# Kernel optimization log

Hardware: AMD Instinct MI355X
Metric: run time of the kernel (lower is better)

Reference implementation:

```python
import jax, jax.numpy as jnp
import numpy as np

B, D, T = 32, 1024, 1000
LMAX = 200
VOCAB = 80
BLANK = VOCAB - 1
NEG = -1e30


def setup_inputs() -> dict:
    key = jax.random.key(0)
    ks = jax.random.split(key, 8)
    decoder_outputs = jax.random.normal(ks[0], (B, D, T), dtype=jnp.float32)
    target_text = jax.random.randint(ks[1], (B, LMAX), 0, BLANK, dtype=jnp.int32)
    decoder_lengths = jax.random.randint(ks[2], (B,), T // 2, T + 1, dtype=jnp.int32)
    target_lengths = jax.random.randint(ks[3], (B,), 1, LMAX + 1, dtype=jnp.int32)
    # learned params (dropout is identity in eval / deterministic reference)
    W1 = jax.random.normal(ks[4], (D, D), dtype=jnp.float32) * (1.0 / np.sqrt(D))
    b1 = jnp.zeros((D,), dtype=jnp.float32)
    W2 = jax.random.normal(ks[5], (D, VOCAB), dtype=jnp.float32) * (1.0 / np.sqrt(D))
    b2 = jnp.zeros((VOCAB,), dtype=jnp.float32)
    return {"decoder_outputs": decoder_outputs, "target_text": target_text,
            "decoder_lengths": decoder_lengths, "target_lengths": target_lengths,
            "W1": W1, "b1": b1, "W2": W2, "b2": b2}


def _ctc_nll(log_probs, targets, input_lengths, target_lengths):
    # log_probs: [T, B, V]; standard CTC alpha (forward) DP over extended labels.
    Tt, Bb, V = log_probs.shape
    L = targets.shape[1]
    S = 2 * L + 1
    ext = jnp.full((Bb, S), BLANK, dtype=targets.dtype).at[:, 1::2].set(targets)
    ext_m2 = jnp.pad(ext, ((0, 0), (2, 0)), constant_values=BLANK)[:, :S]
    allow_skip = (ext != BLANK) & (ext != ext_m2)
    allow_skip = allow_skip.at[:, :2].set(False)

    lp0 = log_probs[0]  # [B, V]
    alpha0 = jnp.full((Bb, S), NEG, dtype=log_probs.dtype)
    alpha0 = alpha0.at[:, 0].set(lp0[:, BLANK])
    alpha0 = alpha0.at[:, 1].set(jnp.take_along_axis(lp0, targets[:, :1], axis=1)[:, 0])

    def step(alpha, inp):
        lp_t, t = inp
        emit = jnp.take_along_axis(lp_t, ext, axis=1)  # [B, S]
        a2 = jnp.pad(alpha, ((0, 0), (1, 0)), constant_values=NEG)[:, :S]
        a3 = jnp.pad(alpha, ((0, 0), (2, 0)), constant_values=NEG)[:, :S]
        a3 = jnp.where(allow_skip, a3, NEG)
        new = jnp.logaddexp(jnp.logaddexp(alpha, a2), a3) + emit
        alpha = jnp.where((t < input_lengths)[:, None], new, alpha)
        return alpha, None

    alpha, _ = jax.lax.scan(step, alpha0, (log_probs[1:], jnp.arange(1, Tt)))
    i1 = (2 * target_lengths - 1)[:, None]
    i2 = (2 * target_lengths)[:, None]
    last = jnp.logaddexp(jnp.take_along_axis(alpha, i1, axis=1)[:, 0],
                         jnp.take_along_axis(alpha, i2, axis=1)[:, 0])
    nll = -last
    # zero_infinity=True: invalid alignments -> 0 loss
    return jnp.where(last > NEG / 2, nll, 0.0)


def reference(decoder_outputs, target_text, decoder_lengths, target_lengths, W1, b1, W2, b2):
    x = jnp.transpose(decoder_outputs, (0, 2, 1))          # [B, T, D]
    h = jax.nn.relu(jnp.einsum('btd,de->bte', x, W1) + b1)  # proj + ReLU (dropout=identity)
    logits = jnp.einsum('btd,dv->btv', h, W2) + b2          # [B, T, V]
    log_probs = jax.nn.log_softmax(logits, axis=2)
    log_probs = jnp.transpose(log_probs, (1, 0, 2))         # [T, B, V]
    ctc_loss = _ctc_nll(log_probs, target_text, decoder_lengths, target_lengths)
    return (ctc_loss / decoder_lengths.astype(jnp.float32)).mean()
```

## Files before the change

kernel.cpp:

```cpp
#include <hip/hip_runtime.h>
#include <cstdint>
#include <cstddef>

#define BN_ 32
#define DD_ 1024
#define TT_ 1000
#define LMAX_ 200
#define VC_ 80
#define BLANK_ 79
#define SS_ 401
#define SPAD 512
#define NEGV (-1e30f)

typedef _Float16 half8 __attribute__((ext_vector_type(8)));
typedef float f32x4 __attribute__((ext_vector_type(4)));

__device__ __forceinline__ void async16(const void* g, void* l) {
  __builtin_amdgcn_global_load_lds(
      (const __attribute__((address_space(1))) unsigned int*)g,
      (__attribute__((address_space(3))) unsigned int*)l, 16, 0, 0);
}

__global__ void transpose_cast_kernel(const float* __restrict__ in,
                                      _Float16* __restrict__ out,
                                      int R, int C) {
  __shared__ float tile[32][33];
  size_t bo = (size_t)blockIdx.z * R * C;
  int c0 = blockIdx.x * 32, r0 = blockIdx.y * 32;
  int tx = threadIdx.x, ty = threadIdx.y;
#pragma unroll
  for (int k = 0; k < 32; k += 8) {
    int r = r0 + ty + k, c = c0 + tx;
    if (r < R && c < C) tile[ty + k][tx] = in[bo + (size_t)r * C + c];
  }
  __syncthreads();
#pragma unroll
  for (int k = 0; k < 32; k += 8) {
    int c = c0 + ty + k, r = r0 + tx;
    if (c < C && r < R) out[bo + (size_t)c * R + r] = (_Float16)tile[tx][ty + k];
  }
}

__global__ __launch_bounds__(256) void gemm_relu_kernel(
    const _Float16* __restrict__ A, const _Float16* __restrict__ Bt,
    const float* __restrict__ bias, _Float16* __restrict__ H,
    int M, int N, int K) {
  constexpr int BK = 64;
  __shared__ __align__(16) _Float16 sA[128 * BK];
  __shared__ __align__(16) _Float16 sB[128 * BK];
  int tid = threadIdx.x;
  int wave = tid >> 6, lane = tid & 63;
  int quad = lane >> 4, r16 = lane & 15;
  int m0 = blockIdx.y * 128, n0 = blockIdx.x * 128;
  int moff = (wave >> 1) * 64, noff = (wave & 1) * 64;

  f32x4 acc[4][4];
#pragma unroll
  for (int i = 0; i < 4; ++i)
#pragma unroll
    for (int j = 0; j < 4; ++j) acc[i][j] = {0.f, 0.f, 0.f, 0.f};

  for (int kt = 0; kt < K; kt += BK) {
#pragma unroll
    for (int jj = 0; jj < 4; ++jj) {
      int seg = tid + 256 * jj;
      int row = seg >> 3, slot = seg & 7;
      int cg = slot ^ (row & 7);
      async16(A + (size_t)(m0 + row) * K + kt + cg * 8, &sA[seg * 8]);
      async16(Bt + (size_t)(n0 + row) * K + kt + cg * 8, &sB[seg * 8]);
    }
    __syncthreads();
#pragma unroll
    for (int ku = 0; ku < 2; ++ku) {
      int sw = ((ku * 4 + quad) ^ (r16 & 7)) * 8;
      half8 af[4], bfr[4];
#pragma unroll
      for (int i = 0; i < 4; ++i)
        af[i] = *(const half8*)&sA[(moff + i * 16 + r16) * BK + sw];
#pragma unroll
      for (int j = 0; j < 4; ++j)
        bfr[j] = *(const half8*)&sB[(noff + j * 16 + r16) * BK + sw];
#pragma unroll
      for (int i = 0; i < 4; ++i)
#pragma unroll
        for (int j = 0; j < 4; ++j)
          acc[i][j] = __builtin_amdgcn_mfma_f32_16x16x32_f16(af[i], bfr[j], acc[i][j], 0, 0, 0);
    }
    __syncthreads();
  }
#pragma unroll
  for (int j = 0; j < 4; ++j) {
    int n = n0 + noff + j * 16 + r16;
    float bv = bias[n];
#pragma unroll
    for (int i = 0; i < 4; ++i) {
#pragma unroll
      for (int r = 0; r < 4; ++r) {
        int m = m0 + moff + i * 16 + quad * 4 + r;
        float v = acc[i][j][r] + bv;
        v = fmaxf(v, 0.f);
        H[(size_t)m * N + n] = (_Float16)v;
      }
    }
  }
}

__global__ __launch_bounds__(256) void gemm_lsm_kernel(
    const _Float16* __restrict__ A, const _Float16* __restrict__ Bt,
    const float* __restrict__ bias, float* __restrict__ LP, int M, int K) {
  constexpr int BK = 64;
  __shared__ __align__(16) _Float16 sA[128 * BK];
  __shared__ __align__(16) _Float16 sB[VC_ * BK];
  int tid = threadIdx.x;
  int wave = tid >> 6, lane = tid & 63;
  int quad = lane >> 4, r16 = lane & 15;
  int m0 = blockIdx.x * 128;

  f32x4 acc[2][5];
#pragma unroll
  for (int i = 0; i < 2; ++i)
#pragma unroll
    for (int j = 0; j < 5; ++j) acc[i][j] = {0.f, 0.f, 0.f, 0.f};

  for (int kt = 0; kt < K; kt += BK) {
#pragma unroll
    for (int jj = 0; jj < 4; ++jj) {
      int seg = tid + 256 * jj;
      int row = seg >> 3, slot = seg & 7;
      int cg = slot ^ (row & 7);
      async16(A + (size_t)(m0 + row) * K + kt + cg * 8, &sA[seg * 8]);
    }
#pragma unroll
    for (int jj = 0; jj < 3; ++jj) {
      int seg = tid + 256 * jj;
      if (seg < VC_ * 8) {
        int row = seg >> 3, slot = seg & 7;
        int cg = slot ^ (row & 7);
        async16(Bt + (size_t)row * K + kt + cg * 8, &sB[seg * 8]);
      }
    }
    __syncthreads();
#pragma unroll
    for (int ku = 0; ku < 2; ++ku) {
      int sw = ((ku * 4 + quad) ^ (r16 & 7)) * 8;
      half8 af[2], bfr[5];
#pragma unroll
      for (int i = 0; i < 2; ++i)
        af[i] = *(const half8*)&sA[(wave * 32 + i * 16 + r16) * BK + sw];
#pragma unroll
      for (int j = 0; j < 5; ++j)
        bfr[j] = *(const half8*)&sB[(j * 16 + r16) * BK + sw];
#pragma unroll
      for (int i = 0; i < 2; ++i)
#pragma unroll
        for (int j = 0; j < 5; ++j)
          acc[i][j] = __builtin_amdgcn_mfma_f32_16x16x32_f16(af[i], bfr[j], acc[i][j], 0, 0, 0);
    }
    __syncthreads();
  }
  float bv[5];
#pragma unroll
  for (int j = 0; j < 5; ++j) bv[j] = bias[j * 16 + r16];
#pragma unroll
  for (int i = 0; i < 2; ++i) {
#pragma unroll
    for (int rr = 0; rr < 4; ++rr) {
      float vals[5];
      float mx = -3.4e38f;
#pragma unroll
      for (int j = 0; j < 5; ++j) {
        vals[j] = acc[i][j][rr] + bv[j];
        mx = fmaxf(mx, vals[j]);
      }
#pragma unroll
      for (int d = 1; d < 16; d <<= 1) mx = fmaxf(mx, __shfl_xor(mx, d));
      float sm = 0.f;
#pragma unroll
      for (int j = 0; j < 5; ++j) sm += expf(vals[j] - mx);
#pragma unroll
      for (int d = 1; d < 16; d <<= 1) sm += __shfl_xor(sm, d);
      float lse = mx + logf(sm);
      int m = m0 + wave * 32 + i * 16 + quad * 4 + rr;
      float* o = LP + (size_t)m * VC_;
#pragma unroll
      for (int j = 0; j < 5; ++j) o[j * 16 + r16] = vals[j] - lse;
    }
  }
}

__global__ __launch_bounds__(256) void emit_kernel(
    const float* __restrict__ LP, const int* __restrict__ targets,
    float* __restrict__ EM) {
  int idx = blockIdx.x * 256 + threadIdx.x;
  int s = idx & (SPAD - 1);
  int bt = idx >> 9;
  float v = 0.f;
  if (s < SS_) {
    int lab = BLANK_;
    if (s & 1) {
      int b = bt / TT_;
      lab = targets[b * LMAX_ + (s >> 1)];
    }
    v = __expf(LP[(size_t)bt * VC_ + lab]);
  }
  EM[idx] = v;
}

__device__ __forceinline__ void dp_step_fwd(float (&bta)[8], int& k,
                                            const f32x4 e0, const f32x4 e1,
                                            const float (&am)[4], int lane) {
  float pm1 = __shfl_up(bta[7], 1);
  int pk = __shfl_up(k, 1);
  if (lane == 0) { pm1 = 0.f; pk = k; }
  int knew = max(k, pk);
  pm1 = ldexpf(pm1, pk - knew);
  int ds = k - knew;
#pragma unroll
  for (int r = 0; r < 8; ++r) bta[r] = ldexpf(bta[r], ds);
  k = knew;
  float nb[8];
  nb[0] = (bta[0] + pm1) * e0.x;
  nb[1] = fmaf(am[0], pm1, bta[1] + bta[0]) * e0.y;
  nb[2] = (bta[2] + bta[1]) * e0.z;
  nb[3] = fmaf(am[1], bta[1], bta[3] + bta[2]) * e0.w;
  nb[4] = (bta[4] + bta[3]) * e1.x;
  nb[5] = fmaf(am[2], bta[3], bta[5] + bta[4]) * e1.y;
  nb[6] = (bta[6] + bta[5]) * e1.z;
  nb[7] = fmaf(am[3], bta[5], bta[7] + bta[6]) * e1.w;
#pragma unroll
  for (int r = 0; r < 8; ++r) bta[r] = nb[r];
}

__device__ __forceinline__ void dp_step_bwd(float (&g)[8], int& k,
                                            const f32x4 e0, const f32x4 e1,
                                            const float (&amB)[4], int lane) {
  float gh[8];
  gh[0] = g[0] * e0.x; gh[1] = g[1] * e0.y;
  gh[2] = g[2] * e0.z; gh[3] = g[3] * e0.w;
  gh[4] = g[4] * e1.x; gh[5] = g[5] * e1.y;
  gh[6] = g[6] * e1.z; gh[7] = g[7] * e1.w;
  float qm1 = __shfl_down(gh[0], 1);
  float qm2 = __shfl_down(gh[1], 1);
  int nk = __shfl_down(k, 1);
  if (lane == 63) { qm1 = 0.f; qm2 = 0.f; nk = k; }
  int knew = max(k, nk);
  int dq = nk - knew;
  qm1 = ldexpf(qm1, dq);
  qm2 = ldexpf(qm2, dq);
  int ds = k - knew;
#pragma unroll
  for (int r = 0; r < 8; ++r) gh[r] = ldexpf(gh[r], ds);
  k = knew;
  g[0] = gh[0] + gh[1];
  g[1] = fmaf(amB[0], gh[3], gh[1] + gh[2]);
  g[2] = gh[2] + gh[3];
  g[3] = fmaf(amB[1], gh[5], gh[3] + gh[4]);
  g[4] = gh[4] + gh[5];
  g[5] = fmaf(amB[2], gh[7], gh[5] + gh[6]);
  g[6] = gh[6] + gh[7];
  g[7] = fmaf(amB[3], qm2, gh[7] + qm1);
}

__device__ __forceinline__ void dp_rescale(float (&v)[8], int& k) {
  float m = fmaxf(fmaxf(fmaxf(v[0], v[1]), fmaxf(v[2], v[3])),
                  fmaxf(fmaxf(v[4], v[5]), fmaxf(v[6], v[7])));
  int ex = (__float_as_int(m) >> 23) - 126;
  k += ex;
#pragma unroll
  for (int r = 0; r < 8; ++r) v[r] = ldexpf(v[r], -ex);
}

__device__ __forceinline__ float allow_f(const int* __restrict__ tg, int s) {
  if (!(s & 1) || s < 3) return 0.f;
  int li = s >> 1;
  if (li >= LMAX_) return 0.f;
  int lab = tg[li];
  return (lab != BLANK_ && lab != tg[li - 1]) ? 1.f : 0.f;
}

__global__ __launch_bounds__(128) void ctc_dp_kernel(
    const float* __restrict__ EM, const int* __restrict__ targets,
    const int* __restrict__ dlen, const int* __restrict__ tlen,
    float* __restrict__ partial) {
  __shared__ float sg[SPAD];
  __shared__ int skg[64];
  int b = blockIdx.x;
  int wave = threadIdx.x >> 6;
  int lane = threadIdx.x & 63;
  const float* em = EM + (size_t)b * TT_ * SPAD + lane * 8;
  const int* tg = targets + b * LMAX_;
  int Tl = dlen[b], Ll = tlen[b];
  int tm = Tl >> 1;

  constexpr int PD = 8;
  f32x4 pf[PD][2];
  float v[8];
  int k = 0;

  if (wave == 0) {
    float am[4];
#pragma unroll
    for (int j = 0; j < 4; ++j) am[j] = allow_f(tg, lane * 8 + 2 * j + 1);
    f32x4 r0a = *(const f32x4*)(em);
#pragma unroll
    for (int r = 0; r < 8; ++r) v[r] = 0.f;
    if (lane == 0) { v[0] = r0a.x; v[1] = r0a.y; }
#pragma unroll
    for (int j = 0; j < PD; ++j) {
      int ri = min(1 + j, TT_ - 1);
      pf[j][0] = *(const f32x4*)(em + (size_t)ri * SPAD);
      pf[j][1] = *(const f32x4*)(em + (size_t)ri * SPAD + 4);
    }
    int t = 1;
    for (; t + (PD - 1) <= tm; t += PD) {
#pragma unroll
      for (int u = 0; u < PD; ++u) {
        dp_step_fwd(v, k, pf[u][0], pf[u][1], am, lane);
        if (u & 1) dp_rescale(v, k);
        int ri = min(t + u + PD, TT_ - 1);
        pf[u][0] = *(const f32x4*)(em + (size_t)ri * SPAD);
        pf[u][1] = *(const f32x4*)(em + (size_t)ri * SPAD + 4);
      }
    }
#pragma unroll
    for (int u = 0; u < PD; ++u) {
      if (t + u <= tm) {
        dp_step_fwd(v, k, pf[u][0], pf[u][1], am, lane);
        if (u & 1) dp_rescale(v, k);
      }
    }
  } else {
    float amB[4];
#pragma unroll
    for (int j = 0; j < 4; ++j) amB[j] = allow_f(tg, lane * 8 + 2 * j + 3);
    int s1 = 2 * Ll - 1, s2 = 2 * Ll;
#pragma unroll
    for (int r = 0; r < 8; ++r) {
      int s = lane * 8 + r;
      v[r] = (s == s1 || s == s2) ? 1.f : 0.f;
    }
#pragma unroll
    for (int j = 0; j < PD; ++j) {
      int ri = max(Tl - 1 - j, 0);
      pf[j][0] = *(const f32x4*)(em + (size_t)ri * SPAD);
      pf[j][1] = *(const f32x4*)(em + (size_t)ri * SPAD + 4);
    }
    int t = Tl - 1;
    for (; t - (PD - 1) > tm; t -= PD) {
#pragma unroll
      for (int u = 0; u < PD; ++u) {
        dp_step_bwd(v, k, pf[u][0], pf[u][1], amB, lane);
        if (u & 1) dp_rescale(v, k);
        int ri = max(t - u - PD, 0);
        pf[u][0] = *(const f32x4*)(em + (size_t)ri * SPAD);
        pf[u][1] = *(const f32x4*)(em + (size_t)ri * SPAD + 4);
      }
    }
#pragma unroll
    for (int u = 0; u < PD; ++u) {
      if (t - u > tm) {
        dp_step_bwd(v, k, pf[u][0], pf[u][1], amB, lane);
        if (u & 1) dp_rescale(v, k);
      }
    }
#pragma unroll
    for (int r = 0; r < 8; ++r) sg[lane * 8 + r] = v[r];
    skg[lane] = k;
  }
  __syncthreads();
  if (wave == 0) {
    float p = 0.f;
#pragma unroll
    for (int r = 0; r < 8; ++r) p = fmaf(v[r], sg[lane * 8 + r], p);
    int kk = k + skg[lane];
    if (p == 0.f) kk = -(1 << 30);
#pragma unroll
    for (int d = 1; d < 64; d <<= 1) {
      float po = __shfl_xor(p, d);
      int ko = __shfl_xor(kk, d);
      int km = max(kk, ko);
      p = ldexpf(p, kk - km) + ldexpf(po, ko - km);
      kk = km;
    }
    if (lane == 0) {
      float nll = 0.f;
      if (p > 0.f) nll = -((log2f(p) + (float)kk) * 0.69314718055994531f);
      partial[b] = nll / (float)Tl;
    }
  }
}

__global__ void finalize_kernel(const float* __restrict__ partial,
                                float* __restrict__ out) {
  int l = threadIdx.x;
  float v = (l < BN_) ? partial[l] : 0.f;
#pragma unroll
  for (int d = 1; d < 64; d <<= 1) v += __shfl_xor(v, d);
  if (l == 0) out[0] = v * (1.f / BN_);
}

extern "C" void kernel_launch(void* const* d_in, const int* in_sizes, int n_in,
                              void* d_out, int out_size, void* d_ws, size_t ws_size,
                              hipStream_t stream) {
  const float* dec = (const float*)d_in[0];
  const int* tgt   = (const int*)d_in[1];
  const int* dln   = (const int*)d_in[2];
  const int* tln   = (const int*)d_in[3];
  const float* W1  = (const float*)d_in[4];
  const float* b1  = (const float*)d_in[5];
  const float* W2  = (const float*)d_in[6];
  const float* b2  = (const float*)d_in[7];
  float* out = (float*)d_out;

  char* ws = (char*)d_ws;
  const size_t M = (size_t)BN_ * TT_;
  _Float16* Af   = (_Float16*)(ws);
  float* EM      = (float*)(ws);
  _Float16* Hf   = (_Float16*)(ws + 65536000);
  _Float16* W1T  = (_Float16*)(ws + 131072000);
  _Float16* W2T  = (_Float16*)(ws + 133169152);
  float* LPp     = (float*)(ws + 133332992);
  float* partial = (float*)(ws + 143572992);

  dim3 tb(32, 8, 1);
  transpose_cast_kernel<<<dim3((TT_ + 31) / 32, DD_ / 32, BN_), tb, 0, stream>>>(dec, Af, DD_, TT_);
  transpose_cast_kernel<<<dim3(DD_ / 32, DD_ / 32, 1), tb, 0, stream>>>(W1, W1T, DD_, DD_);
  transpose_cast_kernel<<<dim3((VC_ + 31) / 32, DD_ / 32, 1), tb, 0, stream>>>(W2, W2T, DD_, VC_);

  gemm_relu_kernel<<<dim3(DD_ / 128, M / 128, 1), 256, 0, stream>>>(
      Af, W1T, b1, Hf, (int)M, DD_, DD_);
  gemm_lsm_kernel<<<dim3(M / 128, 1, 1), 256, 0, stream>>>(
      Hf, W2T, b2, LPp, (int)M, DD_);
  emit_kernel<<<dim3((BN_ * TT_ * SPAD) / 256, 1, 1), 256, 0, stream>>>(LPp, tgt, EM);
  ctc_dp_kernel<<<dim3(BN_, 1, 1), 128, 0, stream>>>(EM, tgt, dln, tln, partial);
  finalize_kernel<<<1, 64, 0, stream>>>(partial, out);
}
```

Before: 453.5 us.

## Merge transposes, shrink LSM GEMM tile, emit probabilities, fold finalize into atomics

```diff
diff --git a/kernel.cpp b/kernel.cpp
--- a/kernel.cpp
+++ b/kernel.cpp
@@ -21,23 +21,43 @@
       (__attribute__((address_space(3))) unsigned int*)l, 16, 0, 0);
 }
 
-__global__ void transpose_cast_kernel(const float* __restrict__ in,
-                                      _Float16* __restrict__ out,
-                                      int R, int C) {
-  __shared__ float tile[32][33];
-  size_t bo = (size_t)blockIdx.z * R * C;
-  int c0 = blockIdx.x * 32, r0 = blockIdx.y * 32;
-  int tx = threadIdx.x, ty = threadIdx.y;
-#pragma unroll
-  for (int k = 0; k < 32; k += 8) {
-    int r = r0 + ty + k, c = c0 + tx;
-    if (r < R && c < C) tile[ty + k][tx] = in[bo + (size_t)r * C + c];
-  }
+__global__ __launch_bounds__(256) void transpose_all_kernel(
+    const float* __restrict__ dec, const float* __restrict__ W1,
+    const float* __restrict__ W2, _Float16* __restrict__ Af,
+    _Float16* __restrict__ W1T, _Float16* __restrict__ W2T) {
+  __shared__ _Float16 T[64][72];
+  int z = blockIdx.z;
+  const float* in; _Float16* out; int C;
+  const int R = 1024;
+  if (z < 32) {
+    in = dec + (size_t)z * R * TT_;
+    out = Af + (size_t)z * TT_ * R;
+    C = TT_;
+  } else if (z == 32) {
+    in = W1; out = W1T; C = 1024;
+  } else {
+    in = W2; out = W2T; C = VC_;
+  }
+  int c0 = blockIdx.x * 64, r0 = blockIdx.y * 64;
+  if (c0 >= C) return;
+  int tid = threadIdx.x;
+  int cl = tid & 63, rg = tid >> 6;
+  int c = c0 + cl;
+  bool cv = (c < C);
+  const float* ip = in + (size_t)(r0 + rg * 16) * C + c;
+  _Float16 h[16];
+#pragma unroll
+  for (int i = 0; i < 16; ++i) h[i] = cv ? (_Float16)ip[(size_t)i * C] : (_Float16)0.f;
+  *(half8*)&T[cl][rg * 16] = *(half8*)&h[0];
+  *(half8*)&T[cl][rg * 16 + 8] = *(half8*)&h[8];
   __syncthreads();
-#pragma unroll
-  for (int k = 0; k < 32; k += 8) {
-    int c = c0 + ty + k, r = r0 + tx;
-    if (c < C && r < R) out[bo + (size_t)c * R + r] = (_Float16)tile[tx][ty + k];
+  int cr = tid >> 2, rc = (tid & 3) * 16;
+  if (c0 + cr < C) {
+    half8 a = *(const half8*)&T[cr][rc];
+    half8 b2 = *(const half8*)&T[cr][rc + 8];
+    _Float16* op = out + (size_t)(c0 + cr) * R + r0 + rc;
+    *(half8*)op = a;
+    *(half8*)(op + 8) = b2;
   }
 }
 
@@ -105,26 +125,24 @@
   }
 }
 
-__global__ __launch_bounds__(256) void gemm_lsm_kernel(
+__global__ __launch_bounds__(256) void gemm_prob_kernel(
     const _Float16* __restrict__ A, const _Float16* __restrict__ Bt,
-    const float* __restrict__ bias, float* __restrict__ LP, int M, int K) {
+    const float* __restrict__ bias, float* __restrict__ P, int M, int K) {
   constexpr int BK = 64;
-  __shared__ __align__(16) _Float16 sA[128 * BK];
+  __shared__ __align__(16) _Float16 sA[64 * BK];
   __shared__ __align__(16) _Float16 sB[VC_ * BK];
   int tid = threadIdx.x;
   int wave = tid >> 6, lane = tid & 63;
   int quad = lane >> 4, r16 = lane & 15;
-  int m0 = blockIdx.x * 128;
-
-  f32x4 acc[2][5];
-#pragma unroll
-  for (int i = 0; i < 2; ++i)
-#pragma unroll
-    for (int j = 0; j < 5; ++j) acc[i][j] = {0.f, 0.f, 0.f, 0.f};
+  int m0 = blockIdx.x * 64;
+
+  f32x4 acc[5];
+#pragma unroll
+  for (int j = 0; j < 5; ++j) acc[j] = {0.f, 0.f, 0.f, 0.f};
 
   for (int kt = 0; kt < K; kt += BK) {
 #pragma unroll
-    for (int jj = 0; jj < 4; ++jj) {
+    for (int jj = 0; jj < 2; ++jj) {
       int seg = tid + 256 * jj;
       int row = seg >> 3, slot = seg & 7;
       int cg = slot ^ (row & 7);
@@ -143,18 +161,14 @@
 #pragma unroll
     for (int ku = 0; ku < 2; ++ku) {
       int sw = ((ku * 4 + quad) ^ (r16 & 7)) * 8;
-      half8 af[2], bfr[5];
-#pragma unroll
-      for (int i = 0; i < 2; ++i)
-        af[i] = *(const half8*)&sA[(wave * 32 + i * 16 + r16) * BK + sw];
+      half8 af = *(const half8*)&sA[(wave * 16 + r16) * BK + sw];
+      half8 bfr[5];
 #pragma unroll
       for (int j = 0; j < 5; ++j)
         bfr[j] = *(const half8*)&sB[(j * 16 + r16) * BK + sw];
 #pragma unroll
-      for (int i = 0; i < 2; ++i)
-#pragma unroll
-        for (int j = 0; j < 5; ++j)
-          acc[i][j] = __builtin_amdgcn_mfma_f32_16x16x32_f16(af[i], bfr[j], acc[i][j], 0, 0, 0);
+      for (int j = 0; j < 5; ++j)
+        acc[j] = __builtin_amdgcn_mfma_f32_16x16x32_f16(af, bfr[j], acc[j], 0, 0, 0);
     }
     __syncthreads();
   }
@@ -162,34 +176,31 @@
 #pragma unroll
   for (int j = 0; j < 5; ++j) bv[j] = bias[j * 16 + r16];
 #pragma unroll
-  for (int i = 0; i < 2; ++i) {
-#pragma unroll
-    for (int rr = 0; rr < 4; ++rr) {
-      float vals[5];
-      float mx = -3.4e38f;
-#pragma unroll
-      for (int j = 0; j < 5; ++j) {
-        vals[j] = acc[i][j][rr] + bv[j];
-        mx = fmaxf(mx, vals[j]);
-      }
-#pragma unroll
-      for (int d = 1; d < 16; d <<= 1) mx = fmaxf(mx, __shfl_xor(mx, d));
-      float sm = 0.f;
-#pragma unroll
-      for (int j = 0; j < 5; ++j) sm += expf(vals[j] - mx);
-#pragma unroll
-      for (int d = 1; d < 16; d <<= 1) sm += __shfl_xor(sm, d);
-      float lse = mx + logf(sm);
-      int m = m0 + wave * 32 + i * 16 + quad * 4 + rr;
-      float* o = LP + (size_t)m * VC_;
-#pragma unroll
-      for (int j = 0; j < 5; ++j) o[j * 16 + r16] = vals[j] - lse;
-    }
+  for (int rr = 0; rr < 4; ++rr) {
+    float vals[5];
+    float mx = -3.4e38f;
+#pragma unroll
+    for (int j = 0; j < 5; ++j) {
+      vals[j] = acc[j][rr] + bv[j];
+      mx = fmaxf(mx, vals[j]);
+    }
+#pragma unroll
+    for (int d = 1; d < 16; d <<= 1) mx = fmaxf(mx, __shfl_xor(mx, d));
+    float ex[5], sm = 0.f;
+#pragma unroll
+    for (int j = 0; j < 5; ++j) { ex[j] = __expf(vals[j] - mx); sm += ex[j]; }
+#pragma unroll
+    for (int d = 1; d < 16; d <<= 1) sm += __shfl_xor(sm, d);
+    float rinv = 1.f / sm;
+    int m = m0 + wave * 16 + quad * 4 + rr;
+    float* o = P + (size_t)m * VC_;
+#pragma unroll
+    for (int j = 0; j < 5; ++j) o[j * 16 + r16] = ex[j] * rinv;
   }
 }
 
 __global__ __launch_bounds__(256) void emit_kernel(
-    const float* __restrict__ LP, const int* __restrict__ targets,
+    const float* __restrict__ P, const int* __restrict__ targets,
     float* __restrict__ EM) {
   int idx = blockIdx.x * 256 + threadIdx.x;
   int s = idx & (SPAD - 1);
@@ -201,7 +212,7 @@
       int b = bt / TT_;
       lab = targets[b * LMAX_ + (s >> 1)];
     }
-    v = __expf(LP[(size_t)bt * VC_ + lab]);
+    v = P[(size_t)bt * VC_ + lab];
   }
   EM[idx] = v;
 }
@@ -281,7 +292,7 @@
 __global__ __launch_bounds__(128) void ctc_dp_kernel(
     const float* __restrict__ EM, const int* __restrict__ targets,
     const int* __restrict__ dlen, const int* __restrict__ tlen,
-    float* __restrict__ partial) {
+    float* __restrict__ out) {
   __shared__ float sg[SPAD];
   __shared__ int skg[64];
   int b = blockIdx.x;
@@ -385,18 +396,9 @@
     if (lane == 0) {
       float nll = 0.f;
       if (p > 0.f) nll = -((log2f(p) + (float)kk) * 0.69314718055994531f);
-      partial[b] = nll / (float)Tl;
-    }
-  }
-}
-
-__global__ void finalize_kernel(const float* __restrict__ partial,
-                                float* __restrict__ out) {
-  int l = threadIdx.x;
-  float v = (l < BN_) ? partial[l] : 0.f;
-#pragma unroll
-  for (int d = 1; d < 64; d <<= 1) v += __shfl_xor(v, d);
-  if (l == 0) out[0] = v * (1.f / BN_);
+      atomicAdd(out, nll / (float)Tl * (1.f / BN_));
+    }
+  }
 }
 
 extern "C" void kernel_launch(void* const* d_in, const int* in_sizes, int n_in,
@@ -419,19 +421,16 @@
   _Float16* Hf   = (_Float16*)(ws + 65536000);
   _Float16* W1T  = (_Float16*)(ws + 131072000);
   _Float16* W2T  = (_Float16*)(ws + 133169152);
-  float* LPp     = (float*)(ws + 133332992);
-  float* partial = (float*)(ws + 143572992);
-
-  dim3 tb(32, 8, 1);
-  transpose_cast_kernel<<<dim3((TT_ + 31) / 32, DD_ / 32, BN_), tb, 0, stream>>>(dec, Af, DD_, TT_);
-  transpose_cast_kernel<<<dim3(DD_ / 32, DD_ / 32, 1), tb, 0, stream>>>(W1, W1T, DD_, DD_);
-  transpose_cast_kernel<<<dim3((VC_ + 31) / 32, DD_ / 32, 1), tb, 0, stream>>>(W2, W2T, DD_, VC_);
-
+  float* Pp      = (float*)(ws + 133332992);
+
+  hipMemsetAsync(d_out, 0, sizeof(float), stream);
+
+  transpose_all_kernel<<<dim3(16, 16, 34), 256, 0, stream>>>(
+      dec, W1, W2, Af, W1T, W2T);
   gemm_relu_kernel<<<dim3(DD_ / 128, M / 128, 1), 256, 0, stream>>>(
       Af, W1T, b1, Hf, (int)M, DD_, DD_);
-  gemm_lsm_kernel<<<dim3(M / 128, 1, 1), 256, 0, stream>>>(
-      Hf, W2T, b2, LPp, (int)M, DD_);
-  emit_kernel<<<dim3((BN_ * TT_ * SPAD) / 256, 1, 1), 256, 0, stream>>>(LPp, tgt, EM);
-  ctc_dp_kernel<<<dim3(BN_, 1, 1), 128, 0, stream>>>(EM, tgt, dln, tln, partial);
-  finalize_kernel<<<1, 64, 0, stream>>>(partial, out);
-}
+  gemm_prob_kernel<<<dim3(M / 64, 1, 1), 256, 0, stream>>>(
+      Hf, W2T, b2, Pp, (int)M, DD_);
+  emit_kernel<<<dim3((BN_ * TT_ * SPAD) / 256, 1, 1), 256, 0, stream>>>(Pp, tgt, EM);
+  ctc_dp_kernel<<<dim3(BN_, 1, 1), 128, 0, stream>>>(EM, tgt, dln, tln, out);
+}
```

New measurement: 439.0 us. 3.2% less time.
